# Kernel optimization log

Measured on AMD Instinct MI355X. Metric: run time of the kernel, lower is better.

Reference implementation:

```python
import jax, jax.numpy as jnp
import numpy as np

E, B, N, F, F1D, H, L, H2, PE_DIM = 4, 16384, 1024, 64, 64, 256, 2, 256, 63
TOPK_MEM = 16      # self.top_K: memory retrieval top-k
W0_SIREN = 30.0    # SIREN omega_0 for 'sine' nonlinearity
NUM_FREQ = 10      # PosEncoding num_frequencies
LINE_DIM = 64      # feat_shapes[0]


def _ln(h, g, b):
    m = jnp.mean(h, axis=-1, keepdims=True)
    v = jnp.mean((h - m) ** 2, axis=-1, keepdims=True)
    return (h - m) / jnp.sqrt(v + 1e-5) * g + b


def _pos_enc(coords):
    # NeRF positional encoding: [coords, sin/cos interleaved per coord per freq]
    freqs = 2.0 ** jnp.arange(NUM_FREQ, dtype=coords.dtype)
    scaled = coords[..., None] * freqs * jnp.pi            # (B, 3, NF)
    sc = jnp.stack([jnp.sin(scaled), jnp.cos(scaled)], axis=-1)  # (B, 3, NF, 2)
    return jnp.concatenate([coords, sc.reshape(coords.shape[0], -1)], axis=-1)  # (B, 63)


def _forward(x, lines, mem_k, mem_v, enc_w0, enc_b0, enc_wh, enc_bh, enc_wo, enc_bo,
             ln_g, ln_b, wq, wk, wv, ad_w0, ad_b0, ad_w1, ad_b1, ad_ln_g, ad_ln_b,
             mg_w0, mg_b0, mg_w1, mg_b1, fw0, fb0, fw1, fb1, fw2, fb2, fw3, fb3, route_k):
    coords = x[:, :3]
    # --- 1D line feature interpolation (param_feats) ---
    p = x[:, 3] * (LINE_DIM - 1)
    pf = jnp.floor(p)
    w = p - pf
    il = pf.astype(jnp.int32)
    ih = jnp.clip(pf + 1.0, 0.0, LINE_DIM - 1).astype(jnp.int32)
    f1d = lines[0][:, il] + w * (lines[0][:, ih] - lines[0][:, il])  # (F1D, B)
    param_feats = f1d.T                                              # (B, F1D)

    pe_x = _pos_enc(coords)                                          # (B, 63)
    scale = float(F) ** 0.5

    def expert(ew0, eb0, ewh, ebh, ewo, ebo, wq_e, wk_e, wv_e, mk, mv,
               aw0, ab0, aw1, ab1, ag, ab):
        # SIREN encoder MLP
        h = jnp.sin(W0_SIREN * (pe_x @ ew0 + eb0))
        for l in range(L):
            h = jnp.sin(W0_SIREN * (h @ ewh[l] + ebh[l]))
        mlp_feats = h @ ewo + ebo                          # (B, F)
        q = _ln(mlp_feats, ln_g, ln_b) @ wq_e              # (B, F)
        kp = mk @ wk_e                                     # (N, F) precomputed keys
        vp = mv @ wv_e                                     # (N, F) precomputed values
        scores = q @ kp.T                                  # (B, N)
        _, idx = jax.lax.top_k(scores, TOPK_MEM)           # (B, K)
        k_top = kp[idx]                                    # (B, K, F)
        v_top = vp[idx]                                    # (B, K, F)
        pfe = jnp.broadcast_to(param_feats[:, None, :], (param_feats.shape[0], TOPK_MEM, F1D))
        a = jnp.concatenate([v_top, pfe], axis=-1)         # (B, K, F+F1D)
        a = jax.nn.relu(a @ aw0 + ab0) @ aw1 + ab1
        adapted = v_top + _ln(a, ag, ab)
        attn = jax.nn.softmax(jnp.einsum('bf,bkf->bk', q, k_top) / scale, axis=-1)
        return jnp.einsum('bk,bkf->bf', attn, adapted) + mlp_feats

    # compute every expert densely (vectorized), then gather routed top-k outputs
    all_out = jax.vmap(expert)(enc_w0, enc_b0, enc_wh, enc_bh, enc_wo, enc_bo,
                               wq, wk, wv, mem_k, mem_v,
                               ad_w0, ad_b0, ad_w1, ad_b1, ad_ln_g, ad_ln_b)  # (E, B, F)

    raw_q = jax.nn.relu(coords @ mg_w0 + mg_b0) @ mg_w1 + mg_b1   # manager_net (B, E)
    probs = jnp.clip(jax.nn.softmax(raw_q, axis=-1), 1e-8, None)
    vals, tidx = jax.lax.top_k(probs, route_k)                    # (B, k)
    vals = vals / jnp.sum(vals, axis=-1, keepdims=True)
    gathered = jnp.take_along_axis(jnp.swapaxes(all_out, 0, 1), tidx[..., None], axis=1)  # (B, k, F)
    spatial = jnp.sum(vals[..., None] * gathered, axis=1)         # (B, F)

    h = jax.nn.relu(spatial @ fw0 + fb0)
    h = jax.nn.relu(h @ fw1 + fb1)
    h = jax.nn.relu(h @ fw2 + fb2)
    refined = jax.nn.sigmoid(h @ fw3 + fb3)
    return refined, raw_q


def setup_inputs() -> dict:
    ks = jax.random.split(jax.random.key(0), 24)
    f32 = jnp.float32
    rn = lambda i, shp, s: jax.random.normal(ks[i], shp, f32) * s
    xav = lambda fi, fo: (2.0 / (fi + fo)) ** 0.5
    return {
        'x': jax.random.uniform(ks[0], (B, 4), f32),
        'lines': jax.random.uniform(ks[1], (1, F1D, LINE_DIM), f32, 0.7, 0.8),
        'mem_k': rn(2, (E, N, F), 1.0),
        'mem_v': rn(3, (E, N, F), 1e-3),
        'enc_w0': rn(4, (E, PE_DIM, H), xav(PE_DIM, H)),
        'enc_b0': jnp.zeros((E, H), f32),
        'enc_wh': rn(5, (E, L, H, H), xav(H, H)),
        'enc_bh': jnp.zeros((E, L, H), f32),
        'enc_wo': rn(6, (E, H, F), xav(H, F)),
        'enc_bo': jnp.zeros((E, F), f32),
        'ln_g': jnp.ones((F,), f32),
        'ln_b': jnp.zeros((F,), f32),
        'wq': rn(7, (E, F, F), xav(F, F)),
        'wk': rn(8, (E, F, F), xav(F, F)),
        'wv': rn(9, (E, F, F), xav(F, F)),
        'ad_w0': rn(10, (E, F + F1D, 64), xav(F + F1D, 64)),
        'ad_b0': rn(11, (E, 64), 1e-3),
        'ad_w1': rn(12, (E, 64, F), xav(64, F)),
        'ad_b1': rn(13, (E, F), 1e-3),
        'ad_ln_g': jnp.ones((E, F), f32),
        'ad_ln_b': jnp.zeros((E, F), f32),
        'mg_w0': rn(14, (3, 64), 0.5),
        'mg_b0': jnp.zeros((64,), f32),
        'mg_w1': rn(15, (64, E), 0.5),
        'mg_b1': jnp.zeros((E,), f32),
        'fw0': rn(16, (F, H2), xav(F, H2)),
        'fb0': rn(17, (H2,), 1e-3),
        'fw1': rn(18, (H2, H2), xav(H2, H2)),
        'fb1': rn(19, (H2,), 1e-3),
        'fw2': rn(20, (H2, H2), xav(H2, H2)),
        'fb2': rn(21, (H2,), 1e-3),
        'fw3': rn(22, (H2, 1), xav(H2, 1)),
        'fb3': rn(23, (1,), 1e-3),
        'route_k': 2,
    }


def reference(x, lines, mem_k, mem_v, enc_w0, enc_b0, enc_wh, enc_bh, enc_wo, enc_bo,
              ln_g, ln_b, wq, wk, wv, ad_w0, ad_b0, ad_w1, ad_b1, ad_ln_g, ad_ln_b,
              mg_w0, mg_b0, mg_w1, mg_b1, fw0, fb0, fw1, fb1, fw2, fb2, fw3, fb3, route_k):
    return _forward(x, lines, mem_k, mem_v, enc_w0, enc_b0, enc_wh, enc_bh, enc_wo, enc_bo,
                    ln_g, ln_b, wq, wk, wv, ad_w0, ad_b0, ad_w1, ad_b1, ad_ln_g, ad_ln_b,
                    mg_w0, mg_b0, mg_w1, mg_b1, fw0, fb0, fw1, fb1, fw2, fb2, fw3, fb3, route_k)
```

## Files before the change

### kernel.cpp

```cpp
#include <hip/hip_runtime.h>
#include <math.h>

#define EE 4
#define BB 16384
#define NN 1024
#define FF 64
#define HH 256
#define PED 63
#define TOPK 16
#define LINE 64
#define TS 32
#define NBX (BB/TS)

#define OFF_KP   0u
#define OFF_VP   262144u
#define OFF_VPA  524288u
#define OFF_PE   786432u
#define OFF_PF   1818624u
#define OFF_EO   2867200u
#define OFF_RW   4964352u
#define OFF_CNT  4997120u
#define OFF_LIST 4997128u
#define OFF_WP   OFF_EO

__device__ __forceinline__ float wred_sum(float v) {
#pragma unroll
    for (int off = 32; off > 0; off >>= 1) v += __shfl_xor(v, off, 64);
    return v;
}
__device__ __forceinline__ void wred_sum2(float& a, float& b) {
#pragma unroll
    for (int off = 32; off > 0; off >>= 1) {
        a += __shfl_xor(a, off, 64);
        b += __shfl_xor(b, off, 64);
    }
}

__global__ __launch_bounds__(256) void k_prep(
    const float* __restrict__ wv, const float* __restrict__ aw0,
    float* __restrict__ wp)
{
    int e = blockIdx.x;
    __shared__ float sa[FF*FF];
    for (int i = threadIdx.x; i < FF*FF; i += 256)
        sa[i] = aw0[(size_t)e*128*FF + i];
    __syncthreads();
    int f = threadIdx.x & 63, dg = threadIdx.x >> 6;
    for (int d = dg; d < FF; d += 4) {
        const float* wr = wv + (size_t)e*FF*FF + d*FF;
        float a = 0.f;
        for (int c = 0; c < FF; ++c) a = fmaf(wr[c], sa[c*FF+f], a);
        wp[(size_t)e*FF*FF + d*FF + f] = a;
    }
}

// ... 82 lines not shown
    for (int j = 0; j < 64; ++j) {
        float h = fmaf(c0, mg_w0[j], fmaf(c1, mg_w0[64+j], fmaf(c2, mg_w0[128+j], mg_b0[j])));
        h = fmaxf(h, 0.f);
#pragma unroll
        for (int e4 = 0; e4 < 4; ++e4) acc[e4] = fmaf(h, mg_w1[j*4+e4], acc[e4]);
    }
#pragma unroll
    for (int e4 = 0; e4 < 4; ++e4) rawq[(size_t)b*4 + e4] = acc[e4];
    float m = fmaxf(fmaxf(acc[0],acc[1]), fmaxf(acc[2],acc[3]));
    float ex[4], den = 0.f;
#pragma unroll
    for (int e4 = 0; e4 < 4; ++e4) { ex[e4] = expf(acc[e4]-m); den += ex[e4]; }
    float pr[4];
#pragma unroll
    for (int e4 = 0; e4 < 4; ++e4) pr[e4] = fmaxf(ex[e4]/den, 1e-8f);
    int i0 = 0;
#pragma unroll
    for (int e4 = 1; e4 < 4; ++e4) if (pr[e4] > pr[i0]) i0 = e4;
    int i1 = -1;
#pragma unroll
    for (int e4 = 0; e4 < 4; ++e4) {
        if (e4 == i0) continue;
        if (i1 < 0 || pr[e4] > pr[i1]) i1 = e4;
    }
    float vs = pr[i0] + pr[i1];
    rw[b*2+0] = pr[i0]/vs;
    rw[b*2+1] = pr[i1]/vs;
    int p0 = atomicAdd(&counts[i0], 1);
    lists[i0*BB + p0] = b*2 + 0;
    int p1 = atomicAdd(&counts[i1], 1);
    lists[i1*BB + p1] = b*2 + 1;
}

__global__ __launch_bounds__(512) void k_expert(
    const float* __restrict__ pe_x, const float* __restrict__ pfm,
    const float* __restrict__ kp, const float* __restrict__ vp,
    const float* __restrict__ vpa,
    const float* __restrict__ enc_w0, const float* __restrict__ enc_b0,
    const float* __restrict__ enc_wh, const float* __restrict__ enc_bh,
    const float* __restrict__ enc_wo, const float* __restrict__ enc_bo,
    const float* __restrict__ ln_g, const float* __restrict__ ln_b,
    const float* __restrict__ wq,
    const float* __restrict__ aw0, const float* __restrict__ ab0,
    const float* __restrict__ aw1, const float* __restrict__ ab1,
    const float* __restrict__ adg, const float* __restrict__ adb,
    const int* __restrict__ counts, const int* __restrict__ lists,
    float* __restrict__ eo)
{
    const int e = blockIdx.y;
    const int base = blockIdx.x * TS;
    const int cnt = counts[e];
    if (base >= cnt) return;

    __shared__ float sh[TS*HH];
    __shared__ float swt[8192];
    __shared__ float wr_l[8*TOPK];
    __shared__ int   tn_l[8*TOPK];
    __shared__ int   slist[TS];

    const int tid = threadIdx.x;
    const int lane = tid & 63;
    const int wv = tid >> 6;
    const int r0 = wv*4;

    if (tid < TS) {
        int idx = base + tid;
        if (idx >= cnt) idx = cnt - 1;
        slist[tid] = lists[e*BB + idx];
    }
    __syncthreads();
    for (int i = tid; i < TS*64; i += 512) {
        int s = i >> 6, j = i & 63;
        int bq = slist[s] >> 1;
        sh[s*HH + j] = (j < PED) ? pe_x[(size_t)bq*PED + j] : 0.f;
    }

    float acc[4][4];

    {
        const float* W = enc_w0 + (size_t)e*PED*HH;
#pragma unroll
        for (int s = 0; s < 4; ++s)
#pragma unroll
            for (int j = 0; j < 4; ++j) acc[s][j] = 0.f;
#pragma unroll 1
        for (int t = 0; t < 2; ++t) {
            int rbase = t*32;
            int rows = (PED - rbase < 32) ? (PED - rbase) : 32;
            int total = rows*HH;
            __syncthreads();
            for (int i = tid*4; i < total; i += 2048)
                *(float4*)&swt[i] = *(const float4*)&W[rbase*HH + i];
            __syncthreads();
#pragma unroll 1
            for (int k = 0; k < rows; ++k) {
                float4 w4 = *(const float4*)&swt[k*HH + 4*lane];
#pragma unroll
                for (int s = 0; s < 4; ++s) {
                    float hv = sh[(r0+s)*HH + rbase + k];
                    acc[s][0] = fmaf(hv, w4.x, acc[s][0]);
                    acc[s][1] = fmaf(hv, w4.y, acc[s][1]);
                    acc[s][2] = fmaf(hv, w4.z, acc[s][2]);
                    acc[s][3] = fmaf(hv, w4.w, acc[s][3]);
                }
            }
        }
        __syncthreads();
        float4 b4 = *(const float4*)&enc_b0[e*HH + 4*lane];
#pragma unroll
        for (int s = 0; s < 4; ++s) {
            float4 o;
            o.x = sinf(30.0f*(acc[s][0] + b4.x));
            o.y = sinf(30.0f*(acc[s][1] + b4.y));
            o.z = sinf(30.0f*(acc[s][2] + b4.z));
            o.w = sinf(30.0f*(acc[s][3] + b4.w));
            *(float4*)&sh[(r0+s)*HH + 4*lane] = o;
        }
    }

#pragma unroll 1
    for (int layer = 0; layer < 2; ++layer) {
        const float* W = enc_wh + ((size_t)(e*2+layer))*HH*HH;
#pragma unroll
        for (int s = 0; s < 4; ++s)
#pragma unroll
            for (int j = 0; j < 4; ++j) acc[s][j] = 0.f;
#pragma unroll 1
        for (int t = 0; t < 8; ++t) {
            __syncthreads();
            for (int i = tid*4; i < 8192; i += 2048)
                *(float4*)&swt[i] = *(const float4*)&W[t*32*HH + i];
            __syncthreads();
#pragma unroll 1
            for (int k4 = 0; k4 < 8; ++k4) {
                float4 h4[4];
#pragma unroll
                for (int s = 0; s < 4; ++s)
                    h4[s] = *(const float4*)&sh[(r0+s)*HH + t*32 + 4*k4];
#pragma unroll
                for (int kk = 0; kk < 4; ++kk) {
                    float4 w4 = *(const float4*)&swt[(4*k4+kk)*HH + 4*lane];
#pragma unroll
                    for (int s = 0; s < 4; ++s) {
                        float hv = (kk==0)?h4[s].x:((kk==1)?h4[s].y:((kk==2)?h4[s].z:h4[s].w));
                        acc[s][0] = fmaf(hv, w4.x, acc[s][0]);
                        acc[s][1] = fmaf(hv, w4.y, acc[s][1]);
                        acc[s][2] = fmaf(hv, w4.z, acc[s][2]);
                        acc[s][3] = fmaf(hv, w4.w, acc[s][3]);
                    }
                }
            }
        }
        __syncthreads();
        float4 b4 = *(const float4*)&enc_bh[(e*2+layer)*HH + 4*lane];
#pragma unroll
        for (int s = 0; s < 4; ++s) {
            float4 o;
            o.x = sinf(30.0f*(acc[s][0] + b4.x));
            o.y = sinf(30.0f*(acc[s][1] + b4.y));
            o.z = sinf(30.0f*(acc[s][2] + b4.z));
            o.w = sinf(30.0f*(acc[s][3] + b4.w));
            *(float4*)&sh[(r0+s)*HH + 4*lane] = o;
        }
    }

    float smlp_r[4];
    {
        const float* W = enc_wo + (size_t)e*HH*FF;
        float a2o[4] = {0.f,0.f,0.f,0.f};
#pragma unroll 1
        for (int t = 0; t < 4; ++t) {
            __syncthreads();
            for (int i = tid*4; i < 4096; i += 2048)
                *(float4*)&swt[i] = *(const float4*)&W[t*64*FF + i];
            __syncthreads();
#pragma unroll 1
            for (int k4 = 0; k4 < 16; ++k4) {
                float4 h4[4];
#pragma unroll
                for (int s = 0; s < 4; ++s)
                    h4[s] = *(const float4*)&sh[(r0+s)*HH + t*64 + 4*k4];
#pragma unroll
                for (int kk = 0; kk < 4; ++kk) {
                    float w = swt[(4*k4+kk)*FF + lane];
#pragma unroll
                    for (int s = 0; s < 4; ++s) {
                        float hv = (kk==0)?h4[s].x:((kk==1)?h4[s].y:((kk==2)?h4[s].z:h4[s].w));
                        a2o[s] = fmaf(hv, w, a2o[s]);
                    }
                }
            }
        }
        float bv = enc_bo[e*FF + lane];
#pragma unroll
        for (int s = 0; s < 4; ++s) smlp_r[s] = a2o[s] + bv;
    }

    {
        const float* Wq = wq + (size_t)e*FF*FF;
        __syncthreads();
        for (int i = tid*4; i < 4096; i += 2048)
            *(float4*)&swt[i] = *(const float4*)&Wq[i];
        __syncthreads();
        float g = ln_g[lane], bb2 = ln_b[lane];
#pragma unroll 1
        for (int s = 0; s < 4; ++s) {
            float hv = smlp_r[s];
            float sm = hv, s2 = hv*hv;
            wred_sum2(sm, s2);
            float mean = sm * (1.f/64.f);
            float var = s2 * (1.f/64.f) - mean*mean;
            float lnv = (hv - mean) * rsqrtf(var + 1e-5f) * g + bb2;
            sh[(r0+s)*HH + lane] = lnv;
            float qa = 0.f;
#pragma unroll 1
            for (int c4 = 0; c4 < 16; ++c4) {
                float4 l4 = *(const float4*)&sh[(r0+s)*HH + 4*c4];
                qa = fmaf(l4.x, swt[(4*c4+0)*FF + lane], qa);
                qa = fmaf(l4.y, swt[(4*c4+1)*FF + lane], qa);
                qa = fmaf(l4.z, swt[(4*c4+2)*FF + lane], qa);
                qa = fmaf(l4.w, swt[(4*c4+3)*FF + lane], qa);
            }
            sh[(r0+s)*HH + 64 + lane] = qa;
        }
    }

    float sc[4][16];
    {
        const float* kpe = kp + (size_t)e*NN*FF;
        const int str = tid >> 3;
        const int stc = (tid & 7) * 8;
#pragma unroll 1
        for (int c = 0; c < 16; ++c) {
            __syncthreads();
            {
                const float* src = kpe + (size_t)(c*64 + str)*FF + stc;
                float* dst = &swt[str*68 + stc];
                *(float4*)(dst+0) = *(const float4*)(src+0);
                *(float4*)(dst+4) = *(const float4*)(src+4);
            }
            __syncthreads();
            float a0 = 0.f, a1 = 0.f, a2s = 0.f, a3 = 0.f;
#pragma unroll
            for (int f4 = 0; f4 < 16; ++f4) {
                float4 k4 = *(const float4*)&swt[lane*68 + 4*f4];
                float4 q0 = *(const float4*)&sh[(r0+0)*HH + 64 + 4*f4];
                float4 q1 = *(const float4*)&sh[(r0+1)*HH + 64 + 4*f4];
                float4 q2 = *(const float4*)&sh[(r0+2)*HH + 64 + 4*f4];
                float4 q3 = *(const float4*)&sh[(r0+3)*HH + 64 + 4*f4];
                a0 = fmaf(k4.x,q0.x,fmaf(k4.y,q0.y,fmaf(k4.z,q0.z,fmaf(k4.w,q0.w,a0))));
                a1 = fmaf(k4.x,q1.x,fmaf(k4.y,q1.y,fmaf(k4.z,q1.z,fmaf(k4.w,q1.w,a1))));
                a2s= fmaf(k4.x,q2.x,fmaf(k4.y,q2.y,fmaf(k4.z,q2.z,fmaf(k4.w,q2.w,a2s))));
                a3 = fmaf(k4.x,q3.x,fmaf(k4.y,q3.y,fmaf(k4.z,q3.z,fmaf(k4.w,q3.w,a3))));
            }
            sc[0][c]=a0; sc[1][c]=a1; sc[2][c]=a2s; sc[3][c]=a3;
        }
    }

    __syncthreads();
    {
        const float* a0bG = aw0 + ((size_t)e*128 + 64)*FF;
        const float* w1G  = aw1 + (size_t)e*FF*FF;
        for (int i = tid*4; i < 4096; i += 2048) {
            *(float4*)&swt[i]        = *(const float4*)&a0bG[i];
            *(float4*)&swt[4096 + i] = *(const float4*)&w1G[i];
        }
    }
    __syncthreads();

    const float* vpe  = vp  + (size_t)e*NN*FF;
    const float* vpae = vpa + (size_t)e*NN*FF;
    const float agv = adg[e*FF + lane], abv = adb[e*FF + lane];
    const float ab1v = ab1[e*FF + lane];
    float* plw = &sh[r0*HH];

#pragma unroll 1
    for (int u = 0; u < 4; ++u) {
        int s = r0 + u;
        int entry = slist[s];
        int bq = entry >> 1;
        float sc_cur[16];
#pragma unroll
        for (int c = 0; c < 16; ++c)
            sc_cur[c] = (u==0)?sc[0][c]:((u==1)?sc[1][c]:((u==2)?sc[2][c]:sc[3][c]));

        float pp = ab0[e*FF + lane];
        {
            const float* pfr = pfm + (size_t)bq*FF;
#pragma unroll 1
            for (int c4 = 0; c4 < 16; ++c4) {
                float4 p4 = *(const float4*)&pfr[4*c4];
                pp = fmaf(p4.x, swt[(4*c4+0)*FF + lane], pp);
                pp = fmaf(p4.y, swt[(4*c4+1)*FF + lane], pp);
                pp = fmaf(p4.z, swt[(4*c4+2)*FF + lane], pp);
                pp = fmaf(p4.w, swt[(4*c4+3)*FF + lane], pp);
            }
        }

        unsigned taken = 0u;
        bool need = true;
        float bv = -1e30f; int bn = 0x7fffffff;
        float v0max = 0.f, wsum = 0.f;
        float parr[16];
#pragma unroll
        for (int r = 0; r < TOPK; ++r) {
            if (need) {
                bv = -1e30f; bn = 0x7fffffff;
#pragma unroll
                for (int c = 0; c < 16; ++c) {
                    float v = sc_cur[c];
                    int n = c*64 + lane;
                    bool ok = !((taken >> c) & 1u);
                    bool better = ok && (v > bv || (v == bv && n < bn));
                    bv = better ? v : bv;
                    bn = better ? n : bn;
                }
                need = false;
            }
            float rv = bv; int rn = bn;
#pragma unroll
            for (int off = 32; off > 0; off >>= 1) {
                float ov = __shfl_xor(rv, off, 64);
                int on = __shfl_xor(rn, off, 64);
                bool better = (ov > rv) || (ov == rv && on < rn);
                rv = better ? ov : rv;
                rn = better ? on : rn;
            }
            if (r == 0) v0max = rv;
            float wr = expf((rv - v0max) * 0.125f);
            wsum += wr;
            if (lane == 0) { wr_l[wv*TOPK + r] = wr; tn_l[wv*TOPK + r] = rn; }
            if ((rn & 63) == lane) { taken |= 1u << (rn >> 6); need = true; }
            parr[r] = fmaxf(vpae[(size_t)rn*FF + lane] + pp, 0.f);
        }
#pragma unroll
        for (int q = 0; q < 4; ++q) {
            int slot = q ^ (lane & 3);
            float4 o; o.x = parr[4*q]; o.y = parr[4*q+1]; o.z = parr[4*q+2]; o.w = parr[4*q+3];
            *(float4*)&plw[lane*16 + slot*4] = o;
        }
        float a2[16];
#pragma unroll
        for (int r = 0; r < 16; ++r) a2[r] = ab1v;
#pragma unroll 1
        for (int j4 = 0; j4 < 16; ++j4) {
            const float* plj = &plw[j4*64];
#pragma unroll
            for (int jj = 0; jj < 4; ++jj) {
                float w = swt[4096 + (4*j4+jj)*FF + lane];
#pragma unroll
                for (int lq = 0; lq < 4; ++lq) {
                    float4 d = *(const float4*)&plj[jj*16 + ((lq ^ jj) * 4)];
                    a2[4*lq+0] = fmaf(d.x, w, a2[4*lq+0]);
                    a2[4*lq+1] = fmaf(d.y, w, a2[4*lq+1]);
                    a2[4*lq+2] = fmaf(d.z, w, a2[4*lq+2]);
                    a2[4*lq+3] = fmaf(d.w, w, a2[4*lq+3]);
                }
            }
        }
        float outacc = 0.f;
#pragma unroll
        for (int r = 0; r < TOPK; ++r) {
            float av = a2[r];
            float sm = av, s2 = av*av;
            wred_sum2(sm, s2);
            float mean = sm * (1.f/64.f);
            float var = s2 * (1.f/64.f) - mean*mean;
            float lnv = (av - mean) * rsqrtf(var + 1e-5f) * agv + abv;
            int n = tn_l[wv*TOPK + r];
            float vt = vpe[(size_t)n*FF + lane];
            outacc = fmaf(wr_l[wv*TOPK + r], vt + lnv, outacc);
        }
        float res = outacc / wsum + smlp_r[u];
        if (base + s < cnt) eo[(size_t)entry*FF + lane] = res;
    }
}

__global__ __launch_bounds__(256) void k_final(
    const float* __restrict__ eo, const float* __restrict__ rw,
    const float* __restrict__ fw0, const float* __restrict__ fb0,
    const float* __restrict__ fw1, const float* __restrict__ fb1,
    const float* __restrict__ fw2, const float* __restrict__ fb2,
    const float* __restrict__ fw3, const float* __restrict__ fb3,
    float* __restrict__ refined)
{
    __shared__ float sh[16*HH];
    const int tid = threadIdx.x, lane = tid & 63, wv = tid >> 6;
    const int sbase = blockIdx.x * 16;
    const int r0 = wv*4;
    for (int i = tid; i < 16*64; i += 256) {
        int s = i >> 6, c = i & 63;
        int b = sbase + s;
        sh[s*HH + c] = rw[b*2]*eo[(size_t)(b*2)*FF + c]
                     + rw[b*2+1]*eo[(size_t)(b*2+1)*FF + c];
    }
    __syncthreads();
    float acc[4][4];
    {
#pragma unroll
        for (int s = 0; s < 4; ++s)
#pragma unroll
            for (int j = 0; j < 4; ++j) acc[s][j] = 0.f;
#pragma unroll 1
        for (int k = 0; k < 64; ++k) {
            float4 w4 = *(const float4*)&fw0[k*HH + 4*lane];
#pragma unroll
            for (int s = 0; s < 4; ++s) {
                float hv = sh[(r0+s)*HH + k];
                acc[s][0] = fmaf(hv, w4.x, acc[s][0]);
                acc[s][1] = fmaf(hv, w4.y, acc[s][1]);
                acc[s][2] = fmaf(hv, w4.z, acc[s][2]);
                acc[s][3] = fmaf(hv, w4.w, acc[s][3]);
            }
        }
        float4 b4 = *(const float4*)&fb0[4*lane];
#pragma unroll
        for (int s = 0; s < 4; ++s) {
            float4 o;
            o.x = fmaxf(acc[s][0] + b4.x, 0.f);
            o.y = fmaxf(acc[s][1] + b4.y, 0.f);
            o.z = fmaxf(acc[s][2] + b4.z, 0.f);
            o.w = fmaxf(acc[s][3] + b4.w, 0.f);
            *(float4*)&sh[(r0+s)*HH + 4*lane] = o;
        }
    }
#pragma unroll 1
    for (int layer = 0; layer < 2; ++layer) {
        const float* W  = layer ? fw2 : fw1;
        const float* bi = layer ? fb2 : fb1;
#pragma unroll
        for (int s = 0; s < 4; ++s)
#pragma unroll
            for (int j = 0; j < 4; ++j) acc[s][j] = 0.f;
#pragma unroll 1
        for (int k4 = 0; k4 < 64; ++k4) {
            float4 h4[4];
#pragma unroll
            for (int s = 0; s < 4; ++s)
                h4[s] = *(const float4*)&sh[(r0+s)*HH + 4*k4];
#pragma unroll
            for (int kk = 0; kk < 4; ++kk) {
                float4 w4 = *(const float4*)&W[(4*k4+kk)*HH + 4*lane];
#pragma unroll
                for (int s = 0; s < 4; ++s) {
                    float hv = (kk==0)?h4[s].x:((kk==1)?h4[s].y:((kk==2)?h4[s].z:h4[s].w));
                    acc[s][0] = fmaf(hv, w4.x, acc[s][0]);
                    acc[s][1] = fmaf(hv, w4.y, acc[s][1]);
                    acc[s][2] = fmaf(hv, w4.z, acc[s][2]);
                    acc[s][3] = fmaf(hv, w4.w, acc[s][3]);
                }
            }
        }
        float4 b4 = *(const float4*)&bi[4*lane];
#pragma unroll
        for (int s = 0; s < 4; ++s) {
            float4 o;
            o.x = fmaxf(acc[s][0] + b4.x, 0.f);
            o.y = fmaxf(acc[s][1] + b4.y, 0.f);
            o.z = fmaxf(acc[s][2] + b4.z, 0.f);
            o.w = fmaxf(acc[s][3] + b4.w, 0.f);
            *(float4*)&sh[(r0+s)*HH + 4*lane] = o;
        }
    }
    {
        float4 w4 = *(const float4*)&fw3[4*lane];
#pragma unroll 1
        for (int s = 0; s < 4; ++s) {
            float4 h4 = *(const float4*)&sh[(r0+s)*HH + 4*lane];
            float part = h4.x*w4.x + h4.y*w4.y + h4.z*w4.z + h4.w*w4.w;
            float tot = wred_sum(part) + fb3[0];
            float r = 1.f/(1.f + expf(-tot));
            if (lane == 0) refined[sbase + r0 + s] = r;
        }
    }
}

extern "C" void kernel_launch(void* const* d_in, const int* in_sizes, int n_in,
                              void* d_out, int out_size, void* d_ws, size_t ws_size,
                              hipStream_t stream)
{
    const float* x      = (const float*)d_in[0];
    const float* lines  = (const float*)d_in[1];
    const float* mem_k  = (const float*)d_in[2];
    const float* mem_v  = (const float*)d_in[3];
    const float* enc_w0 = (const float*)d_in[4];
// ... 7 lines not shown
    const float* wq     = (const float*)d_in[12];
    const float* wk     = (const float*)d_in[13];
    const float* wv_    = (const float*)d_in[14];
    const float* ad_w0  = (const float*)d_in[15];
    const float* ad_b0  = (const float*)d_in[16];
    const float* ad_w1  = (const float*)d_in[17];
    const float* ad_b1  = (const float*)d_in[18];
    const float* ad_g   = (const float*)d_in[19];
    const float* ad_b   = (const float*)d_in[20];
    const float* mg_w0  = (const float*)d_in[21];
    const float* mg_b0  = (const float*)d_in[22];
    const float* mg_w1  = (const float*)d_in[23];
    const float* mg_b1  = (const float*)d_in[24];
    const float* fw0    = (const float*)d_in[25];
    const float* fb0    = (const float*)d_in[26];
    const float* fw1    = (const float*)d_in[27];
    const float* fb1    = (const float*)d_in[28];
    const float* fw2    = (const float*)d_in[29];
    const float* fb2    = (const float*)d_in[30];
    const float* fw3    = (const float*)d_in[31];
    const float* fb3    = (const float*)d_in[32];

    float* out_ref = (float*)d_out;
    float* out_rq  = (float*)d_out + BB;

    float* ws  = (float*)d_ws;
    float* kp  = ws + OFF_KP;
    float* vp  = ws + OFF_VP;
    float* vpa = ws + OFF_VPA;
    float* pe  = ws + OFF_PE;
    float* pfm = ws + OFF_PF;
    float* eo  = ws + OFF_EO;
    float* rw  = ws + OFF_RW;
    float* wpw = ws + OFF_WP;
    int*  cnts = (int*)(ws + OFF_CNT);
    int*  lst  = (int*)(ws + OFF_LIST);

    hipMemsetAsync(cnts, 0, EE*sizeof(int), stream);
    k_prep<<<dim3(EE), dim3(256), 0, stream>>>(wv_, ad_w0, wpw);
    k_proj<<<dim3(EE*64), dim3(256), 0, stream>>>(mem_k, mem_v, wk, wv_, wpw, kp, vp, vpa);
    k_route<<<dim3(BB/256), dim3(256), 0, stream>>>(x, lines, mg_w0, mg_b0, mg_w1, mg_b1,
                                                    pe, pfm, out_rq, rw, cnts, lst);
    k_expert<<<dim3(NBX, EE), dim3(512), 0, stream>>>(pe, pfm, kp, vp, vpa,
        enc_w0, enc_b0, enc_wh, enc_bh, enc_wo, enc_bo, ln_g, ln_b, wq,
        ad_w0, ad_b0, ad_w1, ad_b1, ad_g, ad_b, cnts, lst, eo);
    k_final<<<dim3(BB/16), dim3(256), 0, stream>>>(eo, rw, fw0, fb0, fw1, fb1,
                                                   fw2, fb2, fw3, fb3, out_ref);
}
```

Baseline: 1.485 ms.

## Split expert kernel into MLP and attention kernels to raise occupancy

The monolithic expert kernel becomes two kernels. k_mlp runs the SIREN encoder, layer norm and query projection and writes q and the MLP features to workspace. k_attn does the memory top-k retrieval and the adapter. Each kernel uses less shared memory and gets an explicit launch_bounds occupancy hint, and the weight staging tiles are halved. k_final moves to 32-row, 512-thread blocks that stage fw0 in shared memory. This costs an extra launch and a round trip of q and features through global memory.

```diff
diff --git a/kernel.cpp b/kernel.cpp
--- a/kernel.cpp
+++ b/kernel.cpp
@@ -21,6 +21,8 @@
 #define OFF_RW   4964352u
 #define OFF_CNT  4997120u
 #define OFF_LIST 4997128u
+#define OFF_QV   5062664u
+#define OFF_SM   7159816u
 #define OFF_WP   OFF_EO
 
 __device__ __forceinline__ float wred_sum(float v) {
@@ -169,15 +171,202 @@
     lists[i1*BB + p1] = b*2 + 1;
 }
 
-__global__ __launch_bounds__(512) void k_expert(
-    const float* __restrict__ pe_x, const float* __restrict__ pfm,
-    const float* __restrict__ kp, const float* __restrict__ vp,
-    const float* __restrict__ vpa,
+__global__ __launch_bounds__(512, 6) void k_mlp(
+    const float* __restrict__ pe_x,
     const float* __restrict__ enc_w0, const float* __restrict__ enc_b0,
     const float* __restrict__ enc_wh, const float* __restrict__ enc_bh,
     const float* __restrict__ enc_wo, const float* __restrict__ enc_bo,
     const float* __restrict__ ln_g, const float* __restrict__ ln_b,
     const float* __restrict__ wq,
+    const int* __restrict__ counts, const int* __restrict__ lists,
+    float* __restrict__ qv, float* __restrict__ smlpw)
+{
+    const int e = blockIdx.y;
+    const int base = blockIdx.x * TS;
+    const int cnt = counts[e];
+    if (base >= cnt) return;
+
+    __shared__ float sh[TS*HH];
+    __shared__ float swt[4096];
+    __shared__ int   slist[TS];
+
+    const int tid = threadIdx.x;
+    const int lane = tid & 63;
+    const int wv = tid >> 6;
+    const int r0 = wv*4;
+
+    if (tid < TS) {
+        int idx = base + tid;
+        if (idx >= cnt) idx = cnt - 1;
+        slist[tid] = lists[e*BB + idx];
+    }
+    __syncthreads();
+    for (int i = tid; i < TS*64; i += 512) {
+        int s = i >> 6, j = i & 63;
+        int bq = slist[s] >> 1;
+        sh[s*HH + j] = (j < PED) ? pe_x[(size_t)bq*PED + j] : 0.f;
+    }
+
+    float acc[4][4];
+
+    {
+        const float* W = enc_w0 + (size_t)e*PED*HH;
+#pragma unroll
+        for (int s = 0; s < 4; ++s)
+#pragma unroll
+            for (int j = 0; j < 4; ++j) acc[s][j] = 0.f;
+#pragma unroll 1
+        for (int t = 0; t < 4; ++t) {
+            int rbase = t*16;
+            int rows = (PED - rbase < 16) ? (PED - rbase) : 16;
+            int total = rows*HH;
+            __syncthreads();
+            for (int i = tid*4; i < total; i += 2048)
+                *(float4*)&swt[i] = *(const float4*)&W[rbase*HH + i];
+            __syncthreads();
+#pragma unroll 1
+            for (int k = 0; k < rows; ++k) {
+                float4 w4 = *(const float4*)&swt[k*HH + 4*lane];
+#pragma unroll
+                for (int s = 0; s < 4; ++s) {
+                    float hv = sh[(r0+s)*HH + rbase + k];
+                    acc[s][0] = fmaf(hv, w4.x, acc[s][0]);
+                    acc[s][1] = fmaf(hv, w4.y, acc[s][1]);
+                    acc[s][2] = fmaf(hv, w4.z, acc[s][2]);
+                    acc[s][3] = fmaf(hv, w4.w, acc[s][3]);
+                }
+            }
+        }
+        __syncthreads();
+        float4 b4 = *(const float4*)&enc_b0[e*HH + 4*lane];
+#pragma unroll
+        for (int s = 0; s < 4; ++s) {
+            float4 o;
+            o.x = sinf(30.0f*(acc[s][0] + b4.x));
+            o.y = sinf(30.0f*(acc[s][1] + b4.y));
+            o.z = sinf(30.0f*(acc[s][2] + b4.z));
+            o.w = sinf(30.0f*(acc[s][3] + b4.w));
+            *(float4*)&sh[(r0+s)*HH + 4*lane] = o;
+        }
+    }
+
+#pragma unroll 1
+    for (int layer = 0; layer < 2; ++layer) {
+        const float* W = enc_wh + ((size_t)(e*2+layer))*HH*HH;
+#pragma unroll
+        for (int s = 0; s < 4; ++s)
+#pragma unroll
+            for (int j = 0; j < 4; ++j) acc[s][j] = 0.f;
+#pragma unroll 1
+        for (int t = 0; t < 16; ++t) {
+            __syncthreads();
+            for (int i = tid*4; i < 4096; i += 2048)
+                *(float4*)&swt[i] = *(const float4*)&W[t*16*HH + i];
+            __syncthreads();
+#pragma unroll 1
+            for (int k4 = 0; k4 < 4; ++k4) {
+                float4 h4[4];
+#pragma unroll
+                for (int s = 0; s < 4; ++s)
+                    h4[s] = *(const float4*)&sh[(r0+s)*HH + t*16 + 4*k4];
+#pragma unroll
+                for (int kk = 0; kk < 4; ++kk) {
+                    float4 w4 = *(const float4*)&swt[(4*k4+kk)*HH + 4*lane];
+#pragma unroll
+                    for (int s = 0; s < 4; ++s) {
+                        float hv = (kk==0)?h4[s].x:((kk==1)?h4[s].y:((kk==2)?h4[s].z:h4[s].w));
+                        acc[s][0] = fmaf(hv, w4.x, acc[s][0]);
+                        acc[s][1] = fmaf(hv, w4.y, acc[s][1]);
+                        acc[s][2] = fmaf(hv, w4.z, acc[s][2]);
+                        acc[s][3] = fmaf(hv, w4.w, acc[s][3]);
+                    }
+                }
+            }
+        }
+        __syncthreads();
+        float4 b4 = *(const float4*)&enc_bh[(e*2+layer)*HH + 4*lane];
+#pragma unroll
+        for (int s = 0; s < 4; ++s) {
+            float4 o;
+            o.x = sinf(30.0f*(acc[s][0] + b4.x));
+            o.y = sinf(30.0f*(acc[s][1] + b4.y));
+            o.z = sinf(30.0f*(acc[s][2] + b4.z));
+            o.w = sinf(30.0f*(acc[s][3] + b4.w));
+            *(float4*)&sh[(r0+s)*HH + 4*lane] = o;
+        }
+    }
+
+    float smlp_r[4];
+    {
+        const float* W = enc_wo + (size_t)e*HH*FF;
+        float a2o[4] = {0.f,0.f,0.f,0.f};
+#pragma unroll 1
+        for (int t = 0; t < 4; ++t) {
+            __syncthreads();
+            for (int i = tid*4; i < 4096; i += 2048)
+                *(float4*)&swt[i] = *(const float4*)&W[t*64*FF + i];
+            __syncthreads();
+#pragma unroll 1
+            for (int k4 = 0; k4 < 16; ++k4) {
+                float4 h4[4];
+#pragma unroll
+                for (int s = 0; s < 4; ++s)
+                    h4[s] = *(const float4*)&sh[(r0+s)*HH + t*64 + 4*k4];
+#pragma unroll
+                for (int kk = 0; kk < 4; ++kk) {
+                    float w = swt[(4*k4+kk)*FF + lane];
+#pragma unroll
+                    for (int s = 0; s < 4; ++s) {
+                        float hv = (kk==0)?h4[s].x:((kk==1)?h4[s].y:((kk==2)?h4[s].z:h4[s].w));
+                        a2o[s] = fmaf(hv, w, a2o[s]);
+                    }
+                }
+            }
+        }
+        float bv = enc_bo[e*FF + lane];
+#pragma unroll
+        for (int s = 0; s < 4; ++s) smlp_r[s] = a2o[s] + bv;
+    }
+
+    {
+        const float* Wq = wq + (size_t)e*FF*FF;
+        __syncthreads();
+        for (int i = tid*4; i < 4096; i += 2048)
+            *(float4*)&swt[i] = *(const float4*)&Wq[i];
+        __syncthreads();
+        float g = ln_g[lane], bb2 = ln_b[lane];
+#pragma unroll 1
+        for (int s = 0; s < 4; ++s) {
+            float hv = smlp_r[s];
+            float sm = hv, s2 = hv*hv;
+            wred_sum2(sm, s2);
+            float mean = sm * (1.f/64.f);
+            float var = s2 * (1.f/64.f) - mean*mean;
+            float lnv = (hv - mean) * rsqrtf(var + 1e-5f) * g + bb2;
+            sh[(r0+s)*HH + lane] = lnv;
+            float qa = 0.f;
+#pragma unroll 1
+            for (int c4 = 0; c4 < 16; ++c4) {
+                float4 l4 = *(const float4*)&sh[(r0+s)*HH + 4*c4];
+                qa = fmaf(l4.x, swt[(4*c4+0)*FF + lane], qa);
+                qa = fmaf(l4.y, swt[(4*c4+1)*FF + lane], qa);
+                qa = fmaf(l4.z, swt[(4*c4+2)*FF + lane], qa);
+                qa = fmaf(l4.w, swt[(4*c4+3)*FF + lane], qa);
+            }
+            if (base + r0 + s < cnt) {
+                size_t entry = (size_t)slist[r0+s];
+                qv[entry*FF + lane] = qa;
+                smlpw[entry*FF + lane] = smlp_r[s];
+            }
+        }
+    }
+}
+
+__global__ __launch_bounds__(512, 4) void k_attn(
+    const float* __restrict__ pfm,
+    const float* __restrict__ kp, const float* __restrict__ vp,
+    const float* __restrict__ vpa,
+    const float* __restrict__ qv, const float* __restrict__ smlpw,
     const float* __restrict__ aw0, const float* __restrict__ ab0,
     const float* __restrict__ aw1, const float* __restrict__ ab1,
     const float* __restrict__ adg, const float* __restrict__ adb,
@@ -189,10 +378,10 @@
     const int cnt = counts[e];
     if (base >= cnt) return;
 
-    __shared__ float sh[TS*HH];
     __shared__ float swt[8192];
+    __shared__ float sq[TS*FF];
+    __shared__ float pl[8*1024];
     __shared__ float wr_l[8*TOPK];
-    __shared__ int   tn_l[8*TOPK];
     __shared__ int   slist[TS];
 
     const int tid = threadIdx.x;
@@ -207,34 +396,206 @@
     }
     __syncthreads();
     for (int i = tid; i < TS*64; i += 512) {
-        int s = i >> 6, j = i & 63;
-        int bq = slist[s] >> 1;
-        sh[s*HH + j] = (j < PED) ? pe_x[(size_t)bq*PED + j] : 0.f;
-    }
-
+        int s = i >> 6, c = i & 63;
+        sq[i] = qv[(size_t)slist[s]*FF + c];
+    }
+
+    float sc[4][16];
+    {
+        const float* kpe = kp + (size_t)e*NN*FF;
+        const int str = tid >> 3;
+        const int stc = (tid & 7) * 8;
+#pragma unroll 1
+        for (int c = 0; c < 16; ++c) {
+            __syncthreads();
+            {
+                const float* src = kpe + (size_t)(c*64 + str)*FF + stc;
+                float* dst = &swt[str*68 + stc];
+                *(float4*)(dst+0) = *(const float4*)(src+0);
+                *(float4*)(dst+4) = *(const float4*)(src+4);
+            }
+            __syncthreads();
+            float a0 = 0.f, a1 = 0.f, a2s = 0.f, a3 = 0.f;
+#pragma unroll
+            for (int f4 = 0; f4 < 16; ++f4) {
+                float4 k4 = *(const float4*)&swt[lane*68 + 4*f4];
+                float4 q0 = *(const float4*)&sq[(r0+0)*FF + 4*f4];
+                float4 q1 = *(const float4*)&sq[(r0+1)*FF + 4*f4];
+                float4 q2 = *(const float4*)&sq[(r0+2)*FF + 4*f4];
+                float4 q3 = *(const float4*)&sq[(r0+3)*FF + 4*f4];
+                a0 = fmaf(k4.x,q0.x,fmaf(k4.y,q0.y,fmaf(k4.z,q0.z,fmaf(k4.w,q0.w,a0))));
+                a1 = fmaf(k4.x,q1.x,fmaf(k4.y,q1.y,fmaf(k4.z,q1.z,fmaf(k4.w,q1.w,a1))));
+                a2s= fmaf(k4.x,q2.x,fmaf(k4.y,q2.y,fmaf(k4.z,q2.z,fmaf(k4.w,q2.w,a2s))));
+                a3 = fmaf(k4.x,q3.x,fmaf(k4.y,q3.y,fmaf(k4.z,q3.z,fmaf(k4.w,q3.w,a3))));
+            }
+            sc[0][c]=a0; sc[1][c]=a1; sc[2][c]=a2s; sc[3][c]=a3;
+        }
+    }
+
+    __syncthreads();
+    {
+        const float* a0bG = aw0 + ((size_t)e*128 + 64)*FF;
+        const float* w1G  = aw1 + (size_t)e*FF*FF;
+        for (int i = tid*4; i < 4096; i += 2048) {
+            *(float4*)&swt[i]        = *(const float4*)&a0bG[i];
+            *(float4*)&swt[4096 + i] = *(const float4*)&w1G[i];
+        }
+    }
+    __syncthreads();
+
+    const float* vpe  = vp  + (size_t)e*NN*FF;
+    const float* vpae = vpa + (size_t)e*NN*FF;
+    const float agv = adg[e*FF + lane], abv = adb[e*FF + lane];
+    const float ab0v = ab0[e*FF + lane];
+    const float ab1v = ab1[e*FF + lane];
+    float* plw = &pl[wv*1024];
+
+#pragma unroll
+    for (int u = 0; u < 4; ++u) {
+        int s = r0 + u;
+        int entry = slist[s];
+        int bq = entry >> 1;
+
+        float pp = ab0v;
+        {
+            const float* pfr = pfm + (size_t)bq*FF;
+#pragma unroll 1
+            for (int c4 = 0; c4 < 16; ++c4) {
+                float4 p4 = *(const float4*)&pfr[4*c4];
+                pp = fmaf(p4.x, swt[(4*c4+0)*FF + lane], pp);
+                pp = fmaf(p4.y, swt[(4*c4+1)*FF + lane], pp);
+                pp = fmaf(p4.z, swt[(4*c4+2)*FF + lane], pp);
+                pp = fmaf(p4.w, swt[(4*c4+3)*FF + lane], pp);
+            }
+        }
+
+        int rns[16];
+        unsigned taken = 0u;
+        bool need = true;
+        float bv = -1e30f; int bn = 0x7fffffff;
+        float v0max = 0.f, wsum = 0.f;
+#pragma unroll
+        for (int r = 0; r < TOPK; ++r) {
+            if (need) {
+                bv = -1e30f; bn = 0x7fffffff;
+#pragma unroll
+                for (int c = 0; c < 16; ++c) {
+                    float v = sc[u][c];
+                    int n = c*64 + lane;
+                    bool ok = !((taken >> c) & 1u);
+                    bool better = ok && (v > bv || (v == bv && n < bn));
+                    bv = better ? v : bv;
+                    bn = better ? n : bn;
+                }
+                need = false;
+            }
+            float rv = bv; int rn = bn;
+#pragma unroll
+            for (int off = 32; off > 0; off >>= 1) {
+                float ov = __shfl_xor(rv, off, 64);
+                int on = __shfl_xor(rn, off, 64);
+                bool better = (ov > rv) || (ov == rv && on < rn);
+                rv = better ? ov : rv;
+                rn = better ? on : rn;
+            }
+            if (r == 0) v0max = rv;
+            float wr = expf((rv - v0max) * 0.125f);
+            wsum += wr;
+            if (lane == 0) wr_l[wv*TOPK + r] = wr;
+            if ((rn & 63) == lane) { taken |= 1u << (rn >> 6); need = true; }
+            rns[r] = rn;
+        }
+
+        float pav[16];
+#pragma unroll
+        for (int r = 0; r < TOPK; ++r)
+            pav[r] = vpae[(size_t)rns[r]*FF + lane];
+#pragma unroll
+        for (int q = 0; q < 4; ++q) {
+            int slot = q ^ (lane & 3);
+            float4 o;
+            o.x = fmaxf(pav[4*q+0] + pp, 0.f);
+            o.y = fmaxf(pav[4*q+1] + pp, 0.f);
+            o.z = fmaxf(pav[4*q+2] + pp, 0.f);
+            o.w = fmaxf(pav[4*q+3] + pp, 0.f);
+            *(float4*)&plw[lane*16 + slot*4] = o;
+        }
+        float a2[16];
+#pragma unroll
+        for (int r = 0; r < 16; ++r) a2[r] = ab1v;
+#pragma unroll 1
+        for (int j4 = 0; j4 < 16; ++j4) {
+            const float* plj = &plw[j4*64];
+#pragma unroll
+            for (int jj = 0; jj < 4; ++jj) {
+                float w = swt[4096 + (4*j4+jj)*FF + lane];
+#pragma unroll
+                for (int lq = 0; lq < 4; ++lq) {
+                    float4 d = *(const float4*)&plj[jj*16 + ((lq ^ jj) * 4)];
+                    a2[4*lq+0] = fmaf(d.x, w, a2[4*lq+0]);
+                    a2[4*lq+1] = fmaf(d.y, w, a2[4*lq+1]);
+                    a2[4*lq+2] = fmaf(d.z, w, a2[4*lq+2]);
+                    a2[4*lq+3] = fmaf(d.w, w, a2[4*lq+3]);
+                }
+            }
+        }
+        float vvt[16];
+#pragma unroll
+        for (int r = 0; r < TOPK; ++r)
+            vvt[r] = vpe[(size_t)rns[r]*FF + lane];
+        float outacc = 0.f;
+#pragma unroll
+        for (int r = 0; r < TOPK; ++r) {
+            float av = a2[r];
+            float sm = av, s2 = av*av;
+            wred_sum2(sm, s2);
+            float mean = sm * (1.f/64.f);
+            float var = s2 * (1.f/64.f) - mean*mean;
+            float lnv = (av - mean) * rsqrtf(var + 1e-5f) * agv + abv;
+            outacc = fmaf(wr_l[wv*TOPK + r], vvt[r] + lnv, outacc);
+        }
+        float res = outacc / wsum + smlpw[(size_t)entry*FF + lane];
+        if (base + s < cnt) eo[(size_t)entry*FF + lane] = res;
+    }
+}
+
+__global__ __launch_bounds__(512, 6) void k_final(
+    const float* __restrict__ eo, const float* __restrict__ rw,
+    const float* __restrict__ fw0, const float* __restrict__ fb0,
+    const float* __restrict__ fw1, const float* __restrict__ fb1,
+    const float* __restrict__ fw2, const float* __restrict__ fb2,
+    const float* __restrict__ fw3, const float* __restrict__ fb3,
+    float* __restrict__ refined)
+{
+    __shared__ float sh[TS*HH];
+    __shared__ float swt[4096];
+    const int tid = threadIdx.x, lane = tid & 63, wv = tid >> 6;
+    const int sbase = blockIdx.x * TS;
+    const int r0 = wv*4;
+    for (int i = tid; i < TS*64; i += 512) {
+        int s = i >> 6, c = i & 63;
+        int b = sbase + s;
+        sh[s*HH + c] = rw[b*2]*eo[(size_t)(b*2)*FF + c]
+                     + rw[b*2+1]*eo[(size_t)(b*2+1)*FF + c];
+    }
     float acc[4][4];
-
     {
-        const float* W = enc_w0 + (size_t)e*PED*HH;
 #pragma unroll
         for (int s = 0; s < 4; ++s)
 #pragma unroll
             for (int j = 0; j < 4; ++j) acc[s][j] = 0.f;
 #pragma unroll 1
-        for (int t = 0; t < 2; ++t) {
-            int rbase = t*32;
-            int rows = (PED - rbase < 32) ? (PED - rbase) : 32;
-            int total = rows*HH;
-            __syncthreads();
-            for (int i = tid*4; i < total; i += 2048)
-                *(float4*)&swt[i] = *(const float4*)&W[rbase*HH + i];
-            __syncthreads();
-#pragma unroll 1
-            for (int k = 0; k < rows; ++k) {
+        for (int t = 0; t < 4; ++t) {
+            __syncthreads();
+            for (int i = tid*4; i < 4096; i += 2048)
+                *(float4*)&swt[i] = *(const float4*)&fw0[t*16*HH + i];
+            __syncthreads();
+#pragma unroll 1
+            for (int k = 0; k < 16; ++k) {
                 float4 w4 = *(const float4*)&swt[k*HH + 4*lane];
 #pragma unroll
                 for (int s = 0; s < 4; ++s) {
-                    float hv = sh[(r0+s)*HH + rbase + k];
+                    float hv = sh[(r0+s)*HH + t*16 + k];
                     acc[s][0] = fmaf(hv, w4.x, acc[s][0]);
                     acc[s][1] = fmaf(hv, w4.y, acc[s][1]);
                     acc[s][2] = fmaf(hv, w4.z, acc[s][2]);
@@ -243,37 +604,37 @@
             }
         }
         __syncthreads();
-        float4 b4 = *(const float4*)&enc_b0[e*HH + 4*lane];
+        float4 b4 = *(const float4*)&fb0[4*lane];
 #pragma unroll
         for (int s = 0; s < 4; ++s) {
             float4 o;
-            o.x = sinf(30.0f*(acc[s][0] + b4.x));
-            o.y = sinf(30.0f*(acc[s][1] + b4.y));
-            o.z = sinf(30.0f*(acc[s][2] + b4.z));
-            o.w = sinf(30.0f*(acc[s][3] + b4.w));
+            o.x = fmaxf(acc[s][0] + b4.x, 0.f);
+            o.y = fmaxf(acc[s][1] + b4.y, 0.f);
+            o.z = fmaxf(acc[s][2] + b4.z, 0.f);
+            o.w = fmaxf(acc[s][3] + b4.w, 0.f);
             *(float4*)&sh[(r0+s)*HH + 4*lane] = o;
         }
     }
-
 #pragma unroll 1
     for (int layer = 0; layer < 2; ++layer) {
-        const float* W = enc_wh + ((size_t)(e*2+layer))*HH*HH;
+        const float* W  = layer ? fw2 : fw1;
+        const float* bi = layer ? fb2 : fb1;
 #pragma unroll
         for (int s = 0; s < 4; ++s)
 #pragma unroll
             for (int j = 0; j < 4; ++j) acc[s][j] = 0.f;
 #pragma unroll 1
-        for (int t = 0; t < 8; ++t) {
-            __syncthreads();
-            for (int i = tid*4; i < 8192; i += 2048)
-                *(float4*)&swt[i] = *(const float4*)&W[t*32*HH + i];
-            __syncthreads();
-#pragma unroll 1
-            for (int k4 = 0; k4 < 8; ++k4) {
+        for (int t = 0; t < 16; ++t) {
+            __syncthreads();
+            for (int i = tid*4; i < 4096; i += 2048)
+                *(float4*)&swt[i] = *(const float4*)&W[t*16*HH + i];
+            __syncthreads();
+#pragma unroll 1
+            for (int k4 = 0; k4 < 4; ++k4) {
                 float4 h4[4];
 #pragma unroll
                 for (int s = 0; s < 4; ++s)
-                    h4[s] = *(const float4*)&sh[(r0+s)*HH + t*32 + 4*k4];
+                    h4[s] = *(const float4*)&sh[(r0+s)*HH + t*16 + 4*k4];
 #pragma unroll
                 for (int kk = 0; kk < 4; ++kk) {
                     float4 w4 = *(const float4*)&swt[(4*k4+kk)*HH + 4*lane];
@@ -289,305 +650,6 @@
             }
         }
         __syncthreads();
-        float4 b4 = *(const float4*)&enc_bh[(e*2+layer)*HH + 4*lane];
-#pragma unroll
-        for (int s = 0; s < 4; ++s) {
-            float4 o;
-            o.x = sinf(30.0f*(acc[s][0] + b4.x));
-            o.y = sinf(30.0f*(acc[s][1] + b4.y));
-            o.z = sinf(30.0f*(acc[s][2] + b4.z));
-            o.w = sinf(30.0f*(acc[s][3] + b4.w));
-            *(float4*)&sh[(r0+s)*HH + 4*lane] = o;
-        }
-    }
-
-    float smlp_r[4];
-    {
-        const float* W = enc_wo + (size_t)e*HH*FF;
-        float a2o[4] = {0.f,0.f,0.f,0.f};
-#pragma unroll 1
-        for (int t = 0; t < 4; ++t) {
-            __syncthreads();
-            for (int i = tid*4; i < 4096; i += 2048)
-                *(float4*)&swt[i] = *(const float4*)&W[t*64*FF + i];
-            __syncthreads();
-#pragma unroll 1
-            for (int k4 = 0; k4 < 16; ++k4) {
-                float4 h4[4];
-#pragma unroll
-                for (int s = 0; s < 4; ++s)
-                    h4[s] = *(const float4*)&sh[(r0+s)*HH + t*64 + 4*k4];
-#pragma unroll
-                for (int kk = 0; kk < 4; ++kk) {
-                    float w = swt[(4*k4+kk)*FF + lane];
-#pragma unroll
-                    for (int s = 0; s < 4; ++s) {
-                        float hv = (kk==0)?h4[s].x:((kk==1)?h4[s].y:((kk==2)?h4[s].z:h4[s].w));
-                        a2o[s] = fmaf(hv, w, a2o[s]);
-                    }
-                }
-            }
-        }
-        float bv = enc_bo[e*FF + lane];
-#pragma unroll
-        for (int s = 0; s < 4; ++s) smlp_r[s] = a2o[s] + bv;
-    }
-
-    {
-        const float* Wq = wq + (size_t)e*FF*FF;
-        __syncthreads();
-        for (int i = tid*4; i < 4096; i += 2048)
-            *(float4*)&swt[i] = *(const float4*)&Wq[i];
-        __syncthreads();
-        float g = ln_g[lane], bb2 = ln_b[lane];
-#pragma unroll 1
-        for (int s = 0; s < 4; ++s) {
-            float hv = smlp_r[s];
-            float sm = hv, s2 = hv*hv;
-            wred_sum2(sm, s2);
-            float mean = sm * (1.f/64.f);
-            float var = s2 * (1.f/64.f) - mean*mean;
-            float lnv = (hv - mean) * rsqrtf(var + 1e-5f) * g + bb2;
-            sh[(r0+s)*HH + lane] = lnv;
-            float qa = 0.f;
-#pragma unroll 1
-            for (int c4 = 0; c4 < 16; ++c4) {
-                float4 l4 = *(const float4*)&sh[(r0+s)*HH + 4*c4];
-                qa = fmaf(l4.x, swt[(4*c4+0)*FF + lane], qa);
-                qa = fmaf(l4.y, swt[(4*c4+1)*FF + lane], qa);
-                qa = fmaf(l4.z, swt[(4*c4+2)*FF + lane], qa);
-                qa = fmaf(l4.w, swt[(4*c4+3)*FF + lane], qa);
-            }
-            sh[(r0+s)*HH + 64 + lane] = qa;
-        }
-    }
-
-    float sc[4][16];
-    {
-        const float* kpe = kp + (size_t)e*NN*FF;
-        const int str = tid >> 3;
-        const int stc = (tid & 7) * 8;
-#pragma unroll 1
-        for (int c = 0; c < 16; ++c) {
-            __syncthreads();
-            {
-                const float* src = kpe + (size_t)(c*64 + str)*FF + stc;
-                float* dst = &swt[str*68 + stc];
-                *(float4*)(dst+0) = *(const float4*)(src+0);
-                *(float4*)(dst+4) = *(const float4*)(src+4);
-            }
-            __syncthreads();
-            float a0 = 0.f, a1 = 0.f, a2s = 0.f, a3 = 0.f;
-#pragma unroll
-            for (int f4 = 0; f4 < 16; ++f4) {
-                float4 k4 = *(const float4*)&swt[lane*68 + 4*f4];
-                float4 q0 = *(const float4*)&sh[(r0+0)*HH + 64 + 4*f4];
-                float4 q1 = *(const float4*)&sh[(r0+1)*HH + 64 + 4*f4];
-                float4 q2 = *(const float4*)&sh[(r0+2)*HH + 64 + 4*f4];
-                float4 q3 = *(const float4*)&sh[(r0+3)*HH + 64 + 4*f4];
-                a0 = fmaf(k4.x,q0.x,fmaf(k4.y,q0.y,fmaf(k4.z,q0.z,fmaf(k4.w,q0.w,a0))));
-                a1 = fmaf(k4.x,q1.x,fmaf(k4.y,q1.y,fmaf(k4.z,q1.z,fmaf(k4.w,q1.w,a1))));
-                a2s= fmaf(k4.x,q2.x,fmaf(k4.y,q2.y,fmaf(k4.z,q2.z,fmaf(k4.w,q2.w,a2s))));
-                a3 = fmaf(k4.x,q3.x,fmaf(k4.y,q3.y,fmaf(k4.z,q3.z,fmaf(k4.w,q3.w,a3))));
-            }
-            sc[0][c]=a0; sc[1][c]=a1; sc[2][c]=a2s; sc[3][c]=a3;
-        }
-    }
-
-    __syncthreads();
-    {
-        const float* a0bG = aw0 + ((size_t)e*128 + 64)*FF;
-        const float* w1G  = aw1 + (size_t)e*FF*FF;
-        for (int i = tid*4; i < 4096; i += 2048) {
-            *(float4*)&swt[i]        = *(const float4*)&a0bG[i];
-            *(float4*)&swt[4096 + i] = *(const float4*)&w1G[i];
-        }
-    }
-    __syncthreads();
-
-    const float* vpe  = vp  + (size_t)e*NN*FF;
-    const float* vpae = vpa + (size_t)e*NN*FF;
-    const float agv = adg[e*FF + lane], abv = adb[e*FF + lane];
-    const float ab1v = ab1[e*FF + lane];
-    float* plw = &sh[r0*HH];
-
-#pragma unroll 1
-    for (int u = 0; u < 4; ++u) {
-        int s = r0 + u;
-        int entry = slist[s];
-        int bq = entry >> 1;
-        float sc_cur[16];
-#pragma unroll
-        for (int c = 0; c < 16; ++c)
-            sc_cur[c] = (u==0)?sc[0][c]:((u==1)?sc[1][c]:((u==2)?sc[2][c]:sc[3][c]));
-
-        float pp = ab0[e*FF + lane];
-        {
-            const float* pfr = pfm + (size_t)bq*FF;
-#pragma unroll 1
-            for (int c4 = 0; c4 < 16; ++c4) {
-                float4 p4 = *(const float4*)&pfr[4*c4];
-                pp = fmaf(p4.x, swt[(4*c4+0)*FF + lane], pp);
-                pp = fmaf(p4.y, swt[(4*c4+1)*FF + lane], pp);
-                pp = fmaf(p4.z, swt[(4*c4+2)*FF + lane], pp);
-                pp = fmaf(p4.w, swt[(4*c4+3)*FF + lane], pp);
-            }
-        }
-
-        unsigned taken = 0u;
-        bool need = true;
-        float bv = -1e30f; int bn = 0x7fffffff;
-        float v0max = 0.f, wsum = 0.f;
-        float parr[16];
-#pragma unroll
-        for (int r = 0; r < TOPK; ++r) {
-            if (need) {
-                bv = -1e30f; bn = 0x7fffffff;
-#pragma unroll
-                for (int c = 0; c < 16; ++c) {
-                    float v = sc_cur[c];
-                    int n = c*64 + lane;
-                    bool ok = !((taken >> c) & 1u);
-                    bool better = ok && (v > bv || (v == bv && n < bn));
-                    bv = better ? v : bv;
-                    bn = better ? n : bn;
-                }
-                need = false;
-            }
-            float rv = bv; int rn = bn;
-#pragma unroll
-            for (int off = 32; off > 0; off >>= 1) {
-                float ov = __shfl_xor(rv, off, 64);
-                int on = __shfl_xor(rn, off, 64);
-                bool better = (ov > rv) || (ov == rv && on < rn);
-                rv = better ? ov : rv;
-                rn = better ? on : rn;
-            }
-            if (r == 0) v0max = rv;
-            float wr = expf((rv - v0max) * 0.125f);
-            wsum += wr;
-            if (lane == 0) { wr_l[wv*TOPK + r] = wr; tn_l[wv*TOPK + r] = rn; }
-            if ((rn & 63) == lane) { taken |= 1u << (rn >> 6); need = true; }
-            parr[r] = fmaxf(vpae[(size_t)rn*FF + lane] + pp, 0.f);
-        }
-#pragma unroll
-        for (int q = 0; q < 4; ++q) {
-            int slot = q ^ (lane & 3);
-            float4 o; o.x = parr[4*q]; o.y = parr[4*q+1]; o.z = parr[4*q+2]; o.w = parr[4*q+3];
-            *(float4*)&plw[lane*16 + slot*4] = o;
-        }
-        float a2[16];
-#pragma unroll
-        for (int r = 0; r < 16; ++r) a2[r] = ab1v;
-#pragma unroll 1
-        for (int j4 = 0; j4 < 16; ++j4) {
-            const float* plj = &plw[j4*64];
-#pragma unroll
-            for (int jj = 0; jj < 4; ++jj) {
-                float w = swt[4096 + (4*j4+jj)*FF + lane];
-#pragma unroll
-                for (int lq = 0; lq < 4; ++lq) {
-                    float4 d = *(const float4*)&plj[jj*16 + ((lq ^ jj) * 4)];
-                    a2[4*lq+0] = fmaf(d.x, w, a2[4*lq+0]);
-                    a2[4*lq+1] = fmaf(d.y, w, a2[4*lq+1]);
-                    a2[4*lq+2] = fmaf(d.z, w, a2[4*lq+2]);
-                    a2[4*lq+3] = fmaf(d.w, w, a2[4*lq+3]);
-                }
-            }
-        }
-        float outacc = 0.f;
-#pragma unroll
-        for (int r = 0; r < TOPK; ++r) {
-            float av = a2[r];
-            float sm = av, s2 = av*av;
-            wred_sum2(sm, s2);
-            float mean = sm * (1.f/64.f);
-            float var = s2 * (1.f/64.f) - mean*mean;
-            float lnv = (av - mean) * rsqrtf(var + 1e-5f) * agv + abv;
-            int n = tn_l[wv*TOPK + r];
-            float vt = vpe[(size_t)n*FF + lane];
-            outacc = fmaf(wr_l[wv*TOPK + r], vt + lnv, outacc);
-        }
-        float res = outacc / wsum + smlp_r[u];
-        if (base + s < cnt) eo[(size_t)entry*FF + lane] = res;
-    }
-}
-
-__global__ __launch_bounds__(256) void k_final(
-    const float* __restrict__ eo, const float* __restrict__ rw,
-    const float* __restrict__ fw0, const float* __restrict__ fb0,
-    const float* __restrict__ fw1, const float* __restrict__ fb1,
-    const float* __restrict__ fw2, const float* __restrict__ fb2,
-    const float* __restrict__ fw3, const float* __restrict__ fb3,
-    float* __restrict__ refined)
-{
-    __shared__ float sh[16*HH];
-    const int tid = threadIdx.x, lane = tid & 63, wv = tid >> 6;
-    const int sbase = blockIdx.x * 16;
-    const int r0 = wv*4;
-    for (int i = tid; i < 16*64; i += 256) {
-        int s = i >> 6, c = i & 63;
-        int b = sbase + s;
-        sh[s*HH + c] = rw[b*2]*eo[(size_t)(b*2)*FF + c]
-                     + rw[b*2+1]*eo[(size_t)(b*2+1)*FF + c];
-    }
-    __syncthreads();
-    float acc[4][4];
-    {
-#pragma unroll
-        for (int s = 0; s < 4; ++s)
-#pragma unroll
-            for (int j = 0; j < 4; ++j) acc[s][j] = 0.f;
-#pragma unroll 1
-        for (int k = 0; k < 64; ++k) {
-            float4 w4 = *(const float4*)&fw0[k*HH + 4*lane];
-#pragma unroll
-            for (int s = 0; s < 4; ++s) {
-                float hv = sh[(r0+s)*HH + k];
-                acc[s][0] = fmaf(hv, w4.x, acc[s][0]);
-                acc[s][1] = fmaf(hv, w4.y, acc[s][1]);
-                acc[s][2] = fmaf(hv, w4.z, acc[s][2]);
-                acc[s][3] = fmaf(hv, w4.w, acc[s][3]);
-            }
-        }
-        float4 b4 = *(const float4*)&fb0[4*lane];
-#pragma unroll
-        for (int s = 0; s < 4; ++s) {
-            float4 o;
-            o.x = fmaxf(acc[s][0] + b4.x, 0.f);
-            o.y = fmaxf(acc[s][1] + b4.y, 0.f);
-            o.z = fmaxf(acc[s][2] + b4.z, 0.f);
-            o.w = fmaxf(acc[s][3] + b4.w, 0.f);
-            *(float4*)&sh[(r0+s)*HH + 4*lane] = o;
-        }
-    }
-#pragma unroll 1
-    for (int layer = 0; layer < 2; ++layer) {
-        const float* W  = layer ? fw2 : fw1;
-        const float* bi = layer ? fb2 : fb1;
-#pragma unroll
-        for (int s = 0; s < 4; ++s)
-#pragma unroll
-            for (int j = 0; j < 4; ++j) acc[s][j] = 0.f;
-#pragma unroll 1
-        for (int k4 = 0; k4 < 64; ++k4) {
-            float4 h4[4];
-#pragma unroll
-            for (int s = 0; s < 4; ++s)
-                h4[s] = *(const float4*)&sh[(r0+s)*HH + 4*k4];
-#pragma unroll
-            for (int kk = 0; kk < 4; ++kk) {
-                float4 w4 = *(const float4*)&W[(4*k4+kk)*HH + 4*lane];
-#pragma unroll
-                for (int s = 0; s < 4; ++s) {
-                    float hv = (kk==0)?h4[s].x:((kk==1)?h4[s].y:((kk==2)?h4[s].z:h4[s].w));
-                    acc[s][0] = fmaf(hv, w4.x, acc[s][0]);
-                    acc[s][1] = fmaf(hv, w4.y, acc[s][1]);
-                    acc[s][2] = fmaf(hv, w4.z, acc[s][2]);
-                    acc[s][3] = fmaf(hv, w4.w, acc[s][3]);
-                }
-            }
-        }
         float4 b4 = *(const float4*)&bi[4*lane];
 #pragma unroll
         for (int s = 0; s < 4; ++s) {
@@ -661,6 +723,8 @@
     float* pfm = ws + OFF_PF;
     float* eo  = ws + OFF_EO;
     float* rw  = ws + OFF_RW;
+    float* qvw = ws + OFF_QV;
+    float* smw = ws + OFF_SM;
     float* wpw = ws + OFF_WP;
     int*  cnts = (int*)(ws + OFF_CNT);
     int*  lst  = (int*)(ws + OFF_LIST);
@@ -670,9 +734,11 @@
     k_proj<<<dim3(EE*64), dim3(256), 0, stream>>>(mem_k, mem_v, wk, wv_, wpw, kp, vp, vpa);
     k_route<<<dim3(BB/256), dim3(256), 0, stream>>>(x, lines, mg_w0, mg_b0, mg_w1, mg_b1,
                                                     pe, pfm, out_rq, rw, cnts, lst);
-    k_expert<<<dim3(NBX, EE), dim3(512), 0, stream>>>(pe, pfm, kp, vp, vpa,
+    k_mlp<<<dim3(NBX, EE), dim3(512), 0, stream>>>(pe,
         enc_w0, enc_b0, enc_wh, enc_bh, enc_wo, enc_bo, ln_g, ln_b, wq,
+        cnts, lst, qvw, smw);
+    k_attn<<<dim3(NBX, EE), dim3(512), 0, stream>>>(pfm, kp, vp, vpa, qvw, smw,
         ad_w0, ad_b0, ad_w1, ad_b1, ad_g, ad_b, cnts, lst, eo);
-    k_final<<<dim3(BB/16), dim3(256), 0, stream>>>(eo, rw, fw0, fb0, fw1, fb1,
+    k_final<<<dim3(BB/TS), dim3(512), 0, stream>>>(eo, rw, fw0, fb0, fw1, fb1,
                                                    fw2, fb2, fw3, fb3, out_ref);
 }
```

Measured after the change: 1.225 ms. 1.21x faster.
